# Kernel optimization log

Measured on AMD Instinct MI355X. Metric: run time of the kernel, lower is better.

## Reference

```python
import jax, jax.numpy as jnp
import numpy as np

H = 8  # hidden size (hardcoded in the module)


def _lstm_scan(x, Wih, Whh, b):
    """Unidirectional LSTM over x:[B,T,I] with PyTorch gate order (i,f,g,o).
    Wih:[4H,I], Whh:[4H,H], b:[4H] (= b_ih + b_hh). Returns h seq [B,T,H]."""
    B = x.shape[0]
    # Precompute input projections for all timesteps in one GEMM: [T,B,4H]
    xg = jnp.einsum('bti,gi->tbg', x, Wih) + b

    def step(carry, xt):
        h, c = carry
        z = xt + h @ Whh.T
        i, f, g, o = jnp.split(z, 4, axis=-1)
        c = jax.nn.sigmoid(f) * c + jax.nn.sigmoid(i) * jnp.tanh(g)
        h = jax.nn.sigmoid(o) * jnp.tanh(c)
        return (h, c), h

    init = (jnp.zeros((B, H), x.dtype), jnp.zeros((B, H), x.dtype))
    _, hs = jax.lax.scan(step, init, xg)  # hs: [T,B,H]
    return jnp.swapaxes(hs, 0, 1)


def _bilstm(x, Wih_f, Whh_f, b_f, Wih_b, Whh_b, b_b):
    fwd = _lstm_scan(x, Wih_f, Whh_f, b_f)
    bwd = _lstm_scan(x[:, ::-1], Wih_b, Whh_b, b_b)[:, ::-1]
    return jnp.concatenate([fwd, bwd], axis=-1)  # [B,T,2H]


def setup_inputs() -> dict:
    key = jax.random.key(0)
    ks = jax.random.split(key, 17)
    s = 1.0 / np.sqrt(H)  # PyTorch uniform(-1/sqrt(H), 1/sqrt(H)) init

    def u(k, shape):
        return jax.random.uniform(k, shape, jnp.float32, -s, s)

    x = jax.random.normal(ks[0], (256, 4096, 8), jnp.float32)
    inp = {'x': x}
    # LSTM params: biases are b_ih + b_hh fused (mathematically identical)
    names = [('Wih1f', (4 * H, 8)), ('Whh1f', (4 * H, H)), ('b1f', (4 * H,)),
             ('Wih1b', (4 * H, 8)), ('Whh1b', (4 * H, H)), ('b1b', (4 * H,)),
             ('Wih2f', (4 * H, 8)), ('Whh2f', (4 * H, H)), ('b2f', (4 * H,)),
             ('Wih2b', (4 * H, 8)), ('Whh2b', (4 * H, H)), ('b2b', (4 * H,)),
             ('W1', (8, 2 * H)), ('bl1', (8,)),
             ('W2', (8, 2 * H)), ('bl2', (8,))]
    for i, (name, shape) in enumerate(names):
        inp[name] = u(ks[i + 1], shape)
    return inp


def reference(x, Wih1f, Whh1f, b1f, Wih1b, Whh1b, b1b,
              Wih2f, Whh2f, b2f, Wih2b, Whh2b, b2b,
              W1, bl1, W2, bl2):
    h1 = _bilstm(x, Wih1f, Whh1f, b1f, Wih1b, Whh1b, b1b)   # [B,T,16]
    y1 = h1 @ W1.T + bl1                                     # [B,T,8]
    h2 = _bilstm(y1, Wih2f, Whh2f, b2f, Wih2b, Whh2b, b2b)  # [B,T,16]
    return h2 @ W2.T + bl2                                   # [B,T,8]
```

## Files before the change

kernel.cpp:

```cpp
#include <hip/hip_runtime.h>

#define T_LEN 4096
#define B_SZ  256

typedef float v2f __attribute__((ext_vector_type(2)));
typedef float v4f __attribute__((ext_vector_type(4)));

__device__ __forceinline__ float fexp2(float x) { return __builtin_amdgcn_exp2f(x); }
__device__ __forceinline__ float frcp(float x)  { return __builtin_amdgcn_rcpf(x); }

template<int S>
__device__ __forceinline__ float rorN(float v) {
    return __int_as_float(__builtin_amdgcn_update_dpp(
        0, __float_as_int(v), 0x120 + S, 0xf, 0xf, true));
}

template<int OFF>
__device__ __forceinline__ v4f aload(const float* p) {
    v4f r;
    asm volatile("global_load_dwordx4 %0, %1, off offset:%2"
                 : "=v"(r) : "v"(p), "i"(OFF) : "memory");
    return r;
}
__device__ __forceinline__ void aatomic(float* p, float v) {
    unsafeAtomicAdd(p, v);
}
__device__ __forceinline__ void astore(float* p, float v) {
    asm volatile("global_store_dword %0, %1, off" :: "v"(p), "v"(v) : "memory");
}

__global__ void init_bias_kernel(const float* __restrict__ bl1,
                                 const float* __restrict__ bl2,
                                 float* __restrict__ y1,
                                 float* __restrict__ out)
{
    const long idx = (long)blockIdx.x * blockDim.x + threadIdx.x;
    float4 a1 = make_float4(bl1[0], bl1[1], bl1[2], bl1[3]);
    float4 b1 = make_float4(bl1[4], bl1[5], bl1[6], bl1[7]);
    float4 a2 = make_float4(bl2[0], bl2[1], bl2[2], bl2[3]);
    float4 b2 = make_float4(bl2[4], bl2[5], bl2[6], bl2[7]);
    float4* y4 = (float4*)y1;
    float4* o4 = (float4*)out;
    y4[idx * 2 + 0] = a1;
    y4[idx * 2 + 1] = b1;
    o4[idx * 2 + 0] = a2;
    o4[idx * 2 + 1] = b2;
}

__global__ void proj_kernel(const float* __restrict__ Hf,
                            const float* Hb,
                            const float* __restrict__ W,
                            const float* __restrict__ bl,
                            float* yo)
{
    const long idx = (long)blockIdx.x * blockDim.x + threadIdx.x;
    const float4* f4 = (const float4*)(Hf + idx * 8);
    const float4* b4 = (const float4*)(Hb + idx * 8);
    float4 fa = f4[0], fb = f4[1];
    float4 ba = b4[0], bb = b4[1];
    float o[8];
    #pragma unroll
    for (int d = 0; d < 8; ++d) {
        float s = bl[d];
        s = fmaf(fa.x, W[d * 16 + 0], s);
        s = fmaf(fa.y, W[d * 16 + 1], s);
        s = fmaf(fa.z, W[d * 16 + 2], s);
        s = fmaf(fa.w, W[d * 16 + 3], s);
        s = fmaf(fb.x, W[d * 16 + 4], s);
        s = fmaf(fb.y, W[d * 16 + 5], s);
        s = fmaf(fb.z, W[d * 16 + 6], s);
        s = fmaf(fb.w, W[d * 16 + 7], s);
        s = fmaf(ba.x, W[d * 16 + 8], s);
        s = fmaf(ba.y, W[d * 16 + 9], s);
        s = fmaf(ba.z, W[d * 16 + 10], s);
        s = fmaf(ba.w, W[d * 16 + 11], s);
        s = fmaf(bb.x, W[d * 16 + 12], s);
        s = fmaf(bb.y, W[d * 16 + 13], s);
        s = fmaf(bb.z, W[d * 16 + 14], s);
        s = fmaf(bb.w, W[d * 16 + 15], s);
        o[d] = s;
    }
    float4* y4 = (float4*)(yo + idx * 8);
    y4[0] = make_float4(o[0], o[1], o[2], o[3]);
    y4[1] = make_float4(o[4], o[5], o[6], o[7]);
}

template<int ST, bool PROJ>
__device__ __forceinline__ void rec_body(
    const float* x,
    const float* Wih,
    const float* Whh,
    const float* bias,
    const float* Wp,
    int dcol,
    float* y,
    float* H,
    int b0)
{
    const int tid  = threadIdx.x;
    const int cl   = tid & 15;
    const int j    = cl & 7;
    const int half = cl >> 3;
    const int b    = b0 + (tid >> 4);

    const int rA = half * 16 + j;
    const int rB = half * 16 + 8 + j;

    const float NL2E = -1.4426950408889634f;
    const float GSC  = 2.0f * NL2E;
    const float sA   = half ? GSC : NL2E;
    const float sB   = NL2E;
    const float aselA = half ? 2.0f : GSC;
    const float bselA = half ? -1.0f : 0.0f;

    v2f Whk[8], Wik[8];
    float Wcp[8];
    #pragma unroll
    for (int s = 0; s < 8; ++s) {
        const int k = (j - s) & 7;
        Whk[s] = (v2f){Whh[rA * 8 + k] * sA, Whh[rB * 8 + k] * sB};
        if constexpr (PROJ)
            Wcp[s] = Wp[j * 16 + dcol + k] * 0.5f;
    }
    #pragma unroll
    for (int k = 0; k < 8; ++k)
        Wik[k] = (v2f){Wih[rA * 8 + k] * sA, Wih[rB * 8 + k] * sB};
    const v2f bpk = (v2f){bias[rA] * sA, bias[rB] * sB};

    const int start = (ST > 0) ? 0 : (T_LEN - 1);
    const float* xp = x + ((long)b * T_LEN + start) * 8;
    float* wp = nullptr;
    float* hp = nullptr;
    if constexpr (PROJ)  wp = y + ((long)b * T_LEN + start) * 8 + j;
    if constexpr (!PROJ) hp = H + ((long)b * T_LEN + start) * 8 + j;

    float sc = 0.0f, h = 0.0f;

    auto step = [&](v4f xa, v4f xb, bool doProj) {
        v2f ipA = bpk;
        ipA = __builtin_elementwise_fma(Wik[0], (v2f){xa.x, xa.x}, ipA);
        ipA = __builtin_elementwise_fma(Wik[1], (v2f){xa.y, xa.y}, ipA);
        ipA = __builtin_elementwise_fma(Wik[2], (v2f){xa.z, xa.z}, ipA);
        ipA = __builtin_elementwise_fma(Wik[3], (v2f){xa.w, xa.w}, ipA);
        v2f ipB = Wik[4] * (v2f){xb.x, xb.x};
        ipB = __builtin_elementwise_fma(Wik[5], (v2f){xb.y, xb.y}, ipB);
        ipB = __builtin_elementwise_fma(Wik[6], (v2f){xb.z, xb.z}, ipB);
        ipB = __builtin_elementwise_fma(Wik[7], (v2f){xb.w, xb.w}, ipB);

        float hr0 = h;
        float hr1 = rorN<1>(h);
        float hr2 = rorN<2>(h);
        float hr3 = rorN<3>(h);
        float hr4 = rorN<4>(h);
        float hr5 = rorN<5>(h);
        float hr6 = rorN<6>(h);
        float hr7 = rorN<7>(h);

        v2f cA = __builtin_elementwise_fma(Whk[0], (v2f){hr0, hr0}, ipA);
        cA = __builtin_elementwise_fma(Whk[1], (v2f){hr1, hr1}, cA);
        v2f cB = __builtin_elementwise_fma(Whk[2], (v2f){hr2, hr2}, ipB);
        cB = __builtin_elementwise_fma(Whk[3], (v2f){hr3, hr3}, cB);
        v2f cC = Whk[4] * (v2f){hr4, hr4};
        cC = __builtin_elementwise_fma(Whk[5], (v2f){hr5, hr5}, cC);
        v2f cD = Whk[6] * (v2f){hr6, hr6};
        cD = __builtin_elementwise_fma(Whk[7], (v2f){hr7, hr7}, cD);
        const v2f z = (cA + cB) + (cC + cD);

        if constexpr (PROJ) {
            if (doProj) {
                float pa = hr0 * Wcp[0];
                pa = fmaf(hr1, Wcp[1], pa);
                pa = fmaf(hr2, Wcp[2], pa);
                pa = fmaf(hr3, Wcp[3], pa);
                pa = fmaf(hr4, Wcp[4], pa);
                pa = fmaf(hr5, Wcp[5], pa);
                pa = fmaf(hr6, Wcp[6], pa);
                pa = fmaf(hr7, Wcp[7], pa);
                aatomic(wp, pa);
                wp += ST * 8;
            }
        }

        const float vA = fmaf(frcp(1.0f + fexp2(z.x)), aselA, bselA);
        const float vB = frcp(1.0f + fexp2(z.y));

        const float pAx = rorN<8>(vA);
        const float pBx = rorN<8>(vB);
        const float gf = half ? pBx : vB;
        const float go = half ? vB  : pBx;

        sc = fmaf(gf, sc, vA * pAx);
        const float th = fmaf(frcp(1.0f + fexp2(sc)), 2.0f, -1.0f);
        h = go * th;

        if constexpr (!PROJ) {
            astore(hp, h);
            hp += ST * 8;
        }
    };

    v4f A0, A1, A2, A3, A4, A5, A6, A7;
    v4f B0, B1, B2, B3, B4, B5, B6, B7;
    v4f C0, C1, C2, C3, C4, C5, C6, C7;

#define AREGS A0, A1, A2, A3, A4, A5, A6, A7
#define BREGS B0, B1, B2, B3, B4, B5, B6, B7
#define CREGS C0, C1, C2, C3, C4, C5, C6, C7

#define LOADM_I(P0, P1, P2, P3, P4, P5, P6, P7)                                \
    P0 = aload<0>(xp);            P1 = aload<16>(xp);                          \
    P2 = aload<ST * 32>(xp);      P3 = aload<ST * 32 + 16>(xp);                \
    P4 = aload<ST * 64>(xp);      P5 = aload<ST * 64 + 16>(xp);                \
    P6 = aload<ST * 96>(xp);      P7 = aload<ST * 96 + 16>(xp);                \
    xp += ST * 32;
#define LOADM(REGS) LOADM_I(REGS)

#define WAITM_I(N, P0, P1, P2, P3, P4, P5, P6, P7)                             \
    asm volatile("s_waitcnt vmcnt(" #N ")"                                     \
        : "+v"(P0), "+v"(P1), "+v"(P2), "+v"(P3),                              \
          "+v"(P4), "+v"(P5), "+v"(P6), "+v"(P7) :: "memory")
#define WAITM(N, REGS) WAITM_I(N, REGS)

#define MACRO4_I(P0, P1, P2, P3, P4, P5, P6, P7, FIRSTPROJ)                    \
    step(P0, P1, FIRSTPROJ);                                                   \
    step(P2, P3, true);                                                        \
    step(P4, P5, true);                                                        \
    step(P6, P7, true);
#define MACRO4(REGS, FIRSTPROJ) MACRO4_I(REGS, FIRSTPROJ)

    asm volatile("s_waitcnt vmcnt(0)" ::: "memory");

    LOADM(AREGS)
    LOADM(BREGS)
    LOADM(CREGS)

    if constexpr (PROJ) {
        WAITM(16, AREGS); MACRO4(AREGS, false)
        LOADM(AREGS)
        WAITM(19, BREGS); MACRO4(BREGS, true)
        LOADM(BREGS)
        WAITM(23, CREGS); MACRO4(CREGS, true)
    } else {
        WAITM(16, AREGS); MACRO4(AREGS, true)
        LOADM(AREGS)
        WAITM(20, BREGS); MACRO4(BREGS, true)
        LOADM(BREGS)
        WAITM(24, CREGS); MACRO4(CREGS, true)
    }

    for (int i = 0; i < 339; ++i) {
        LOADM(CREGS) WAITM(24, AREGS); MACRO4(AREGS, true)
        LOADM(AREGS) WAITM(24, BREGS); MACRO4(BREGS, true)
        LOADM(BREGS) WAITM(24, CREGS); MACRO4(CREGS, true)
    }
    LOADM(CREGS)
    WAITM(24, AREGS); MACRO4(AREGS, true)
    LOADM(AREGS)
    WAITM(24, BREGS); MACRO4(BREGS, true)
    WAITM(16, CREGS); MACRO4(CREGS, true)
    WAITM(8,  AREGS); MACRO4(AREGS, true)

#undef LOADM
#undef LOADM_I
#undef MACRO4
#undef MACRO4_I
#undef WAITM
#undef WAITM_I
#undef AREGS
#undef BREGS
#undef CREGS

    if constexpr (PROJ) {
        float pa = h * Wcp[0];
        pa = fmaf(rorN<1>(h), Wcp[1], pa);
        pa = fmaf(rorN<2>(h), Wcp[2], pa);
        pa = fmaf(rorN<3>(h), Wcp[3], pa);
        pa = fmaf(rorN<4>(h), Wcp[4], pa);
        pa = fmaf(rorN<5>(h), Wcp[5], pa);
        pa = fmaf(rorN<6>(h), Wcp[6], pa);
        pa = fmaf(rorN<7>(h), Wcp[7], pa);
        aatomic(wp, pa);
    }
}

__global__ __launch_bounds__(64, 1)
void lstm_rec_kernel(const float* __restrict__ x,
                     const float* __restrict__ WihF, const float* __restrict__ WhhF,
                     const float* __restrict__ bF,
                     const float* __restrict__ WihB, const float* __restrict__ WhhB,
                     const float* __restrict__ bB,
                     const float* __restrict__ Wp,
                     float* __restrict__ y)
{
    if (blockIdx.x < 64)
        rec_body<1,  true>(x, WihF, WhhF, bF, Wp, 0, y, nullptr, 4 * (int)blockIdx.x);
    else
        rec_body<-1, true>(x, WihB, WhhB, bB, Wp, 8, y, nullptr, 4 * ((int)blockIdx.x - 64));
}

__global__ __launch_bounds__(64, 1)
void lstm_rec_np_kernel(const float* __restrict__ x,
                        const float* __restrict__ WihF, const float* __restrict__ WhhF,
                        const float* __restrict__ bF,
                        const float* __restrict__ WihB, const float* __restrict__ WhhB,
                        const float* __restrict__ bB,
                        float* __restrict__ Hf,
                        float* __restrict__ Hb)
{
    if (blockIdx.x < 64)
        rec_body<1,  false>(x, WihF, WhhF, bF, nullptr, 0, nullptr, Hf, 4 * (int)blockIdx.x);
    else
        rec_body<-1, false>(x, WihB, WhhB, bB, nullptr, 0, nullptr, Hb, 4 * ((int)blockIdx.x - 64));
}

extern "C" void kernel_launch(void* const* d_in, const int* in_sizes, int n_in,
                              void* d_out, int out_size, void* d_ws, size_t ws_size,
                              hipStream_t stream)
{
    const float* x     = (const float*)d_in[0];
    const float* Wih1f = (const float*)d_in[1];
    const float* Whh1f = (const float*)d_in[2];
    const float* b1f   = (const float*)d_in[3];
    const float* Wih1b = (const float*)d_in[4];
    const float* Whh1b = (const float*)d_in[5];
    const float* b1b   = (const float*)d_in[6];
    const float* Wih2f = (const float*)d_in[7];
    const float* Whh2f = (const float*)d_in[8];
    const float* b2f   = (const float*)d_in[9];
    const float* Wih2b = (const float*)d_in[10];
    const float* Whh2b = (const float*)d_in[11];
    const float* b2b   = (const float*)d_in[12];
    const float* W1    = (const float*)d_in[13];
    const float* bl1   = (const float*)d_in[14];
    const float* W2    = (const float*)d_in[15];
    const float* bl2   = (const float*)d_in[16];

    float* out = (float*)d_out;
    const int BT = B_SZ * T_LEN;
    const size_t MB32 = (size_t)32 * 1024 * 1024;

    if (ws_size >= 2 * MB32) {
        float* ws0 = (float*)d_ws;
        float* ws1 = (float*)((char*)d_ws + MB32);
        float* Hb  = out;

        lstm_rec_np_kernel<<<128, 64, 0, stream>>>(x, Wih1f, Whh1f, b1f,
                                                   Wih1b, Whh1b, b1b, ws0, Hb);
        proj_kernel<<<BT / 256, 256, 0, stream>>>(ws0, Hb, W1, bl1, ws1);
        lstm_rec_np_kernel<<<128, 64, 0, stream>>>(ws1, Wih2f, Whh2f, b2f,
                                                   Wih2b, Whh2b, b2b, ws0, Hb);
        proj_kernel<<<BT / 256, 256, 0, stream>>>(ws0, Hb, W2, bl2, out);
    } else {
        float* y1 = (float*)d_ws;

        init_bias_kernel<<<BT / 256, 256, 0, stream>>>(bl1, bl2, y1, out);
        lstm_rec_kernel<<<128, 64, 0, stream>>>(x, Wih1f, Whh1f, b1f,
                                                Wih1b, Whh1b, b1b, W1, y1);
        lstm_rec_kernel<<<128, 64, 0, stream>>>(y1, Wih2f, Whh2f, b2f,
                                                Wih2b, Whh2b, b2b, W2, out);
    }
}
```

Baseline: 1.071 ms.

## Precompute LSTM input projections in a parallel kernel before the recurrence

Adds a fully parallel kernel that computes the scaled input-gate projections (Wih·x + b) for all timesteps and both directions into a large workspace. The recurrent kernel then streams these precomputed gates with a triple-buffered asm load pipeline, so the serial per-step critical path only holds the Whh matvec and the activations. The cost is extra global memory traffic (about 128MB of gate data written and read per layer) and a larger workspace requirement. The path is used only when the workspace holds at least 320MB.

```diff
diff --git a/kernel.cpp b/kernel.cpp
--- a/kernel.cpp
+++ b/kernel.cpp
@@ -85,17 +85,192 @@
     y4[1] = make_float4(o[4], o[5], o[6], o[7]);
 }
 
+__global__ __launch_bounds__(256)
+void xg_kernel(const float* __restrict__ x,
+               const float* __restrict__ WihF, const float* __restrict__ bF,
+               const float* __restrict__ WihB, const float* __restrict__ bB,
+               float* __restrict__ xgF, float* __restrict__ xgB)
+{
+    const long per = (long)B_SZ * (T_LEN / 4) * 16;
+    const long gid = (long)blockIdx.x * blockDim.x + threadIdx.x;
+    const int  dir = gid >= per;
+    const long idx = dir ? gid - per : gid;
+    const int  cl  = (int)(idx & 15);
+    const long bt  = idx >> 4;
+    const int  j = cl & 7, half = cl >> 3;
+    const int  rA = half * 16 + j, rB = rA + 8;
+
+    const float NL2E = -1.4426950408889634f;
+    const float GSC  = 2.0f * NL2E;
+    const float sA = half ? GSC : NL2E, sB = NL2E;
+
+    const float* Wih  = dir ? WihB : WihF;
+    const float* bias = dir ? bB : bF;
+    float wa[8], wb[8];
+    #pragma unroll
+    for (int k = 0; k < 8; ++k) {
+        wa[k] = Wih[rA * 8 + k] * sA;
+        wb[k] = Wih[rB * 8 + k] * sB;
+    }
+    const float ba = bias[rA] * sA, bbv = bias[rB] * sB;
+
+    const float* xr = x + bt * 32;
+    float o[8];
+    #pragma unroll
+    for (int s = 0; s < 4; ++s) {
+        const float* xs = xr + s * 8;
+        float zA = ba, zB = bbv;
+        #pragma unroll
+        for (int k = 0; k < 8; ++k) {
+            const float xv = xs[k];
+            zA = fmaf(wa[k], xv, zA);
+            zB = fmaf(wb[k], xv, zB);
+        }
+        o[s * 2 + 0] = zA;
+        o[s * 2 + 1] = zB;
+    }
+    float4* d4 = (float4*)((dir ? xgB : xgF) + idx * 8);
+    d4[0] = make_float4(o[0], o[1], o[2], o[3]);
+    d4[1] = make_float4(o[4], o[5], o[6], o[7]);
+}
+
+template<int ST>
+__device__ __forceinline__ void rec_xg_body(
+    const float* xg,
+    const float* Whh,
+    float* H,
+    int b0)
+{
+    const int tid  = threadIdx.x;
+    const int cl   = tid & 15;
+    const int j    = cl & 7;
+    const int half = cl >> 3;
+    const int b    = b0 + (tid >> 4);
+
+    const int rA = half * 16 + j;
+    const int rB = half * 16 + 8 + j;
+
+    const float NL2E = -1.4426950408889634f;
+    const float GSC  = 2.0f * NL2E;
+    const float sA   = half ? GSC : NL2E;
+    const float sB   = NL2E;
+    const float aselA = half ? 2.0f : GSC;
+    const float bselA = half ? -1.0f : 0.0f;
+
+    v2f Whk[8];
+    #pragma unroll
+    for (int s = 0; s < 8; ++s) {
+        const int k = (j - s) & 7;
+        Whk[s] = (v2f){Whh[rA * 8 + k] * sA, Whh[rB * 8 + k] * sB};
+    }
+
+    const int tb0 = (ST > 0) ? 0 : (T_LEN / 4 - 1);
+    const float* xp = xg + (((long)b * (T_LEN / 4) + tb0) * 16 + cl) * 8;
+    const int t0 = (ST > 0) ? 0 : (T_LEN - 1);
+    float* hp = H + ((long)b * T_LEN + t0) * 8 + j;
+
+    float sc = 0.0f, h = 0.0f;
+
+    auto step = [&](v2f zx) {
+        float hr0 = h;
+        float hr1 = rorN<1>(h);
+        float hr2 = rorN<2>(h);
+        float hr3 = rorN<3>(h);
+        float hr4 = rorN<4>(h);
+        float hr5 = rorN<5>(h);
+        float hr6 = rorN<6>(h);
+        float hr7 = rorN<7>(h);
+
+        v2f cA = __builtin_elementwise_fma(Whk[0], (v2f){hr0, hr0}, zx);
+        cA = __builtin_elementwise_fma(Whk[1], (v2f){hr1, hr1}, cA);
+        v2f cB = Whk[2] * (v2f){hr2, hr2};
+        cB = __builtin_elementwise_fma(Whk[3], (v2f){hr3, hr3}, cB);
+        v2f cC = Whk[4] * (v2f){hr4, hr4};
+        cC = __builtin_elementwise_fma(Whk[5], (v2f){hr5, hr5}, cC);
+        v2f cD = Whk[6] * (v2f){hr6, hr6};
+        cD = __builtin_elementwise_fma(Whk[7], (v2f){hr7, hr7}, cD);
+        const v2f z = (cA + cB) + (cC + cD);
+
+        const float vA = fmaf(frcp(1.0f + fexp2(z.x)), aselA, bselA);
+        const float vB = frcp(1.0f + fexp2(z.y));
+
+        const float pAx = rorN<8>(vA);
+        const float pBx = rorN<8>(vB);
+        const float gf = half ? pBx : vB;
+        const float go = half ? vB  : pBx;
+
+        sc = fmaf(gf, sc, vA * pAx);
+        const float th = fmaf(frcp(1.0f + fexp2(sc)), 2.0f, -1.0f);
+        h = go * th;
+
+        astore(hp, h);
+        hp += ST * 8;
+    };
+
+    v4f A0, A1, B0, B1, C0, C1;
+
+#define LOADM2(P0, P1)                                                         \
+    P0 = aload<0>(xp); P1 = aload<16>(xp); xp += ST * 128;
+
+#define WAITM2(N, P0, P1)                                                      \
+    asm volatile("s_waitcnt vmcnt(" #N ")"                                     \
+        : "+v"(P0), "+v"(P1) :: "memory")
+
+#define MACRO4X(P0, P1)                                                        \
+    if constexpr (ST > 0) {                                                    \
+        step((v2f){P0.x, P0.y}); step((v2f){P0.z, P0.w});                      \
+        step((v2f){P1.x, P1.y}); step((v2f){P1.z, P1.w});                      \
+    } else {                                                                   \
+        step((v2f){P1.z, P1.w}); step((v2f){P1.x, P1.y});                      \
+        step((v2f){P0.z, P0.w}); step((v2f){P0.x, P0.y});                      \
+    }
+
+    asm volatile("s_waitcnt vmcnt(0)" ::: "memory");
+
+    LOADM2(A0, A1)
+    LOADM2(B0, B1)
+    LOADM2(C0, C1)
+    WAITM2(4, A0, A1);  MACRO4X(A0, A1)
+    LOADM2(A0, A1)
+    WAITM2(8, B0, B1);  MACRO4X(B0, B1)
+    LOADM2(B0, B1)
+    WAITM2(12, C0, C1); MACRO4X(C0, C1)
+
+    for (int i = 0; i < 339; ++i) {
+        LOADM2(C0, C1) WAITM2(12, A0, A1); MACRO4X(A0, A1)
+        LOADM2(A0, A1) WAITM2(12, B0, B1); MACRO4X(B0, B1)
+        LOADM2(B0, B1) WAITM2(12, C0, C1); MACRO4X(C0, C1)
+    }
+    LOADM2(C0, C1)
+    WAITM2(12, A0, A1); MACRO4X(A0, A1)
+    LOADM2(A0, A1)
+    WAITM2(12, B0, B1); MACRO4X(B0, B1)
+    WAITM2(10, C0, C1); MACRO4X(C0, C1)
+    WAITM2(8,  A0, A1); MACRO4X(A0, A1)
+
+#undef LOADM2
+#undef WAITM2
+#undef MACRO4X
+}
+
+__global__ __launch_bounds__(64, 1)
+void lstm_rec_xg_kernel(const float* __restrict__ xgF,
+                        const float* __restrict__ xgB,
+                        const float* __restrict__ WhhF,
+                        const float* __restrict__ WhhB,
+                        float* __restrict__ Hf,
+                        float* __restrict__ Hb)
+{
+    if (blockIdx.x < 64)
+        rec_xg_body<1 >(xgF, WhhF, Hf, 4 * (int)blockIdx.x);
+    else
+        rec_xg_body<-1>(xgB, WhhB, Hb, 4 * ((int)blockIdx.x - 64));
+}
+
 template<int ST, bool PROJ>
 __device__ __forceinline__ void rec_body(
-    const float* x,
-    const float* Wih,
-    const float* Whh,
-    const float* bias,
-    const float* Wp,
-    int dcol,
-    float* y,
-    float* H,
-    int b0)
+    const float* x, const float* Wih, const float* Whh, const float* bias,
+    const float* Wp, int dcol, float* y, float* H, int b0)
 {
     const int tid  = threadIdx.x;
     const int cl   = tid & 15;
@@ -339,7 +514,21 @@
     const int BT = B_SZ * T_LEN;
     const size_t MB32 = (size_t)32 * 1024 * 1024;
 
-    if (ws_size >= 2 * MB32) {
+    if (ws_size >= 10 * MB32) {
+        float* xgF = (float*)d_ws;
+        float* xgB = (float*)((char*)d_ws + 4 * MB32);
+        float* Hf  = (float*)((char*)d_ws + 8 * MB32);
+        float* y1  = (float*)((char*)d_ws + 9 * MB32);
+        float* Hb  = out;
+        const int XGB = (int)(2L * B_SZ * (T_LEN / 4) * 16 / 256);
+
+        xg_kernel<<<XGB, 256, 0, stream>>>(x, Wih1f, b1f, Wih1b, b1b, xgF, xgB);
+        lstm_rec_xg_kernel<<<128, 64, 0, stream>>>(xgF, xgB, Whh1f, Whh1b, Hf, Hb);
+        proj_kernel<<<BT / 256, 256, 0, stream>>>(Hf, Hb, W1, bl1, y1);
+        xg_kernel<<<XGB, 256, 0, stream>>>(y1, Wih2f, b2f, Wih2b, b2b, xgF, xgB);
+        lstm_rec_xg_kernel<<<128, 64, 0, stream>>>(xgF, xgB, Whh2f, Whh2b, Hf, Hb);
+        proj_kernel<<<BT / 256, 256, 0, stream>>>(Hf, Hb, W2, bl2, out);
+    } else if (ws_size >= 2 * MB32) {
         float* ws0 = (float*)d_ws;
         float* ws1 = (float*)((char*)d_ws + MB32);
         float* Hb  = out;
```

After: 1.069 ms. No clear change (-0.2%).
